# Optimization experiments

Measured on AMD Instinct MI355X. Metric: run time of the kernel, lower is better.

## Reference

```python
import jax, jax.numpy as jnp
import numpy as np


def _ln(x, g, b, eps=1e-5):
    m = jnp.mean(x, axis=-1, keepdims=True)
    v = jnp.var(x, axis=-1, keepdims=True)  # biased var, matches torch LayerNorm
    return (x - m) / jnp.sqrt(v + eps) * g + b


def setup_inputs() -> dict:
    key = jax.random.key(0)
    ks = jax.random.split(key, 10)
    B, S, T, D, F = 4, 8, 1024, 768, 16
    inp = {
        "target_hidden": jax.random.normal(ks[0], (B, T, D), jnp.float32),
        "support_hidden": jax.random.normal(ks[1], (B, S, T, D), jnp.float32),
        "support_token_mask": jax.random.bernoulli(ks[2], 0.8, (B, S, T)),
        "support_features": jax.random.normal(ks[3], (B, T, F), jnp.float32),
        # LayerNorm params
        "t_g": jnp.ones((D,), jnp.float32), "t_b": jnp.zeros((D,), jnp.float32),
        "s_g": jnp.ones((D,), jnp.float32), "s_b": jnp.zeros((D,), jnp.float32),
        "o_g": jnp.ones((D,), jnp.float32), "o_b": jnp.zeros((D,), jnp.float32),
        # score MLP: Linear(2D->D), GELU, Linear(D->1)
        "score_w1": jax.random.normal(ks[4], (2 * D, D), jnp.float32) * 0.02,
        "score_b1": jnp.zeros((D,), jnp.float32),
        "score_w2": jax.random.normal(ks[5], (D, 1), jnp.float32) * 0.02,
        "score_b2": jnp.zeros((1,), jnp.float32),
        # gate MLP: Linear(2D+F->D), GELU, Linear(D->1), Sigmoid
        "gate_w1": jax.random.normal(ks[6], (2 * D + F, D), jnp.float32) * 0.02,
        "gate_b1": jnp.zeros((D,), jnp.float32),
        "gate_w2": jax.random.normal(ks[7], (D, 1), jnp.float32) * 0.02,
        "gate_b2": jnp.zeros((1,), jnp.float32),
    }
    return inp


def reference(target_hidden, support_hidden, support_token_mask, support_features,
              t_g, t_b, s_g, s_b, o_g, o_b,
              score_w1, score_b1, score_w2, score_b2,
              gate_w1, gate_b1, gate_w2, gate_b2):
    D = target_hidden.shape[-1]
    mask = support_token_mask  # (B,S,T) bool

    th = _ln(target_hidden, t_g, t_b)        # (B,T,D)
    sh = _ln(support_hidden, s_g, s_b)       # (B,S,T,D)

    # score MLP on concat([target_expanded, support], -1) == split-weight form
    h = (jnp.einsum('btd,df->btf', th, score_w1[:D])[:, None, :, :]
         + jnp.einsum('bstd,df->bstf', sh, score_w1[D:]) + score_b1)  # (B,S,T,D)
    h = jax.nn.gelu(h, approximate=False)
    scores = jnp.einsum('bstd,d->bst', h, score_w2[:, 0]) + score_b2[0]  # (B,S,T)

    scores = jnp.where(mask, scores, -10000.0)
    w = jax.nn.softmax(scores, axis=1)
    w = w * mask.astype(w.dtype)
    w = w / jnp.clip(jnp.sum(w, axis=1, keepdims=True), 1e-8)

    summary = jnp.einsum('bst,bstd->btd', w, sh)  # (B,T,D)
    has_support = jnp.any(mask, axis=1)           # (B,T)
    summary = jnp.where(has_support[..., None], summary, 0.0)

    gcat = jnp.concatenate([th, summary, support_features], axis=-1)  # (B,T,2D+F)
    g = jax.nn.gelu(gcat @ gate_w1 + gate_b1, approximate=False)
    gate = jax.nn.sigmoid(g @ gate_w2 + gate_b2)  # (B,T,1)

    fused = gate * summary + (1.0 - gate) * th    # dropout is identity in eval
    out = _ln(th + fused, o_g, o_b)
    return out, gate.squeeze(-1)
```

## Files before the change

kernel.cpp:

```cpp
#include <hip/hip_runtime.h>
#include <hip/hip_bf16.h>

#define D768 768

typedef __attribute__((ext_vector_type(8))) short short8;
typedef __attribute__((ext_vector_type(4))) float f32x4;

__device__ __forceinline__ unsigned short f2bf(float f){
  union { float f; unsigned u; } v; v.f = f;
  unsigned r = v.u + 0x7FFFu + ((v.u >> 16) & 1u);
  return (unsigned short)(r >> 16);
}
__device__ __forceinline__ float bf2f(unsigned short u){
  union { unsigned u; float f; } v; v.u = ((unsigned)u) << 16;
  return v.f;
}
__device__ __forceinline__ float gelu_f(float x){
  float y = fabsf(x) * 0.7071067811865475f;
  float t = __builtin_amdgcn_rcpf(fmaf(0.3275911f, y, 1.0f));
  float p = fmaf(fmaf(fmaf(fmaf(1.061405429f, t, -1.453152027f), t, 1.421413741f),
                      t, -0.284496736f), t, 0.254829592f) * t;
  float e = __expf(-y * y);
  float erf_abs = fmaf(-p, e, 1.0f);
  float erfv = copysignf(erf_abs, x);
  return 0.5f * x * (1.0f + erfv);
}
__device__ __forceinline__ void gload16(const void* g, void* l){
  __builtin_amdgcn_global_load_lds((const __attribute__((address_space(1))) void*)g,
                                   (__attribute__((address_space(3))) void*)l, 16, 0, 0);
}

__global__ void k_ln(const float* __restrict__ x, const float* __restrict__ g,
                     const float* __restrict__ bia, float* __restrict__ of32,
                     unsigned short* __restrict__ obf, int ldo){
  int row = blockIdx.x;
  int t = threadIdx.x;
  const float* xr = x + (size_t)row * D768;
  float4 v = *(const float4*)(xr + t*4);
  float s  = v.x + v.y + v.z + v.w;
  float ss = v.x*v.x + v.y*v.y + v.z*v.z + v.w*v.w;
  for (int o = 32; o; o >>= 1){ s += __shfl_down(s, o); ss += __shfl_down(ss, o); }
  __shared__ float sb[6];
  int wid = t >> 6;
  if ((t & 63) == 0){ sb[wid] = s; sb[3+wid] = ss; }
  __syncthreads();
  s = sb[0] + sb[1] + sb[2]; ss = sb[3] + sb[4] + sb[5];
  float mean = s * (1.f/768.f);
  float var  = ss * (1.f/768.f) - mean*mean;
  float rstd = rsqrtf(var + 1e-5f);
  float4 gv = *(const float4*)(g + t*4);
  float4 bv = *(const float4*)(bia + t*4);
  float o0 = (v.x-mean)*rstd*gv.x + bv.x;
  float o1 = (v.y-mean)*rstd*gv.y + bv.y;
  float o2 = (v.z-mean)*rstd*gv.z + bv.z;
  float o3 = (v.w-mean)*rstd*gv.w + bv.w;
  if (of32){
    float4 ov; ov.x=o0; ov.y=o1; ov.z=o2; ov.w=o3;
    *(float4*)(of32 + (size_t)row * D768 + t*4) = ov;
  }
  ushort4 ub; ub.x=f2bf(o0); ub.y=f2bf(o1); ub.z=f2bf(o2); ub.w=f2bf(o3);
  *(ushort4*)(obf + (size_t)row * ldo + t*4) = ub;
}

__global__ void k_wtall(const float* __restrict__ sw1, const float* __restrict__ gw1,
                        unsigned short* __restrict__ WtA, unsigned short* __restrict__ WtB,
                        unsigned short* __restrict__ WtG,
                        float* __restrict__ scores, const float* __restrict__ sb2,
                        float* __restrict__ gacc, const float* __restrict__ gb2,
                        const unsigned char* __restrict__ m, int* __restrict__ flag){
  int blk = blockIdx.x;
  if (blk < 128){
    int i = blk * 256 + threadIdx.x;
    if (i < 32768) scores[i] = sb2[0];
    if (i < 4096)  gacc[i]   = gb2[0];
    if (blk == 0){
      __shared__ int s;
      if (threadIdx.x == 0) s = 0;
      __syncthreads();
      int nz = 0;
      for (int j = threadIdx.x; j < 2048; j += 256) nz += (m[4*j+1] != 0);
      atomicAdd(&s, nz);
      __syncthreads();
      if (threadIdx.x == 0) *flag = (s == 0) ? 1 : 0;
    }
    return;
  }
  int tile = blk - 128;
  const float* W; unsigned short* Wt; int Kin, Kpad;
  if (tile < 576)      { W = sw1;                 Wt = WtA; Kin = 768;  Kpad = 768;  }
  else if (tile < 1152){ W = sw1 + 768ull*768;    Wt = WtB; Kin = 768;  Kpad = 768;  tile -= 576; }
  else                 { W = gw1;                 Wt = WtG; Kin = 1552; Kpad = 1568; tile -= 1152; }
  int ntk = Kpad >> 5;
  int k0 = (tile % ntk) << 5, n0 = (tile / ntk) << 5;
  __shared__ float ts[32][33];
  int tx = threadIdx.x & 31, ty = threadIdx.x >> 5;
  #pragma unroll
  for (int r = 0; r < 4; ++r){
    int k = k0 + ty + r*8;
    ts[ty + r*8][tx] = (k < Kin) ? W[(size_t)k * D768 + n0 + tx] : 0.f;
  }
  __syncthreads();
  #pragma unroll
  for (int r = 0; r < 4; ++r){
    int n = n0 + ty + r*8;
    Wt[(size_t)n * Kpad + k0 + tx] = f2bf(ts[tx][ty + r*8]);
  }
}

template<int MODE, int BN>
__launch_bounds__(256)
__global__ void k_gemm(const unsigned short* __restrict__ A, int lda,
                       const unsigned short* __restrict__ Bt, int ldb,
                       int ksteps, int ntn,
                       const float* __restrict__ tproj,
                       const float* __restrict__ b1,
                       const float* __restrict__ w2,
                       float* __restrict__ out){
  constexpr int NJ  = BN / 32;
  constexpr int BCH = BN / 64;
  __shared__ __align__(16) unsigned short As[3][128*32];
  __shared__ __align__(16) unsigned short Bs[3][BN*32];
  const int cpx = gridDim.x >> 3;
  const int logical = ((int)blockIdx.x & 7) * cpx + ((int)blockIdx.x >> 3);
  const int m0 = (logical / ntn) * 128, n0 = (logical % ntn) * BN;
  const int t = threadIdx.x, lane = t & 63, w = t >> 6;
  const int wrow = (w >> 1) * 64, wcol = (w & 1) * (BN/2);
  const int lo16 = lane & 15;
  const int hs = ((lane >> 4) ^ ((lo16 >> 1) & 3)) * 8;
  const int crow = lane >> 2;
  const int cseg = (((lane & 3) ^ ((lane >> 3) & 3)) * 8);
  const unsigned short* ga = A  + (size_t)(m0 + w*32 + crow) * lda + cseg;
  const unsigned short* gb = Bt + (size_t)(n0 + w*(BN/4) + crow) * ldb + cseg;
  f32x4 acc[4][NJ] = {};

#define STAGEK(BUF, KS) do {                                                   \
    const unsigned short* gak_ = ga + (size_t)(KS)*32;                         \
    const unsigned short* gbk_ = gb + (size_t)(KS)*32;                         \
    _Pragma("unroll")                                                          \
    for (int c = 0; c < 2; ++c)                                                \
      gload16(gak_ + (size_t)(c*16)*lda, &As[BUF][w*1024 + c*512]);            \
    _Pragma("unroll")                                                          \
    for (int c = 0; c < BCH; ++c)                                              \
      gload16(gbk_ + (size_t)(c*16)*ldb, &Bs[BUF][w*(BN/4)*32 + c*512]);       \
  } while (0)

#define COMPUTEK(BUF) do {                                                     \
    const unsigned short* pa_ = &As[BUF][(wrow + lo16)*32 + hs];               \
    const unsigned short* pb_ = &Bs[BUF][(wcol + lo16)*32 + hs];               \
    short8 af_[4], bf_[NJ];                                                    \
    _Pragma("unroll")                                                          \
    for (int i = 0; i < 4; ++i) af_[i] = *(const short8*)(pa_ + i*16*32);      \
    _Pragma("unroll")                                                          \
    for (int j = 0; j < NJ; ++j) bf_[j] = *(const short8*)(pb_ + j*16*32);     \
    _Pragma("unroll")                                                          \
    for (int i = 0; i < 4; ++i)                                                \
      _Pragma("unroll")                                                        \
      for (int j = 0; j < NJ; ++j)                                             \
        acc[i][j] = __builtin_amdgcn_mfma_f32_16x16x32_bf16(af_[i], bf_[j], acc[i][j], 0, 0, 0); \
  } while (0)

#define WAITN(n) asm volatile("s_waitcnt vmcnt(" #n ")" ::: "memory")

  {
    int pro = ksteps < 2 ? ksteps : 2;
    for (int p = 0; p < pro; ++p) STAGEK(p, p);
  }
  for (int ks = 0; ks < ksteps; ++ks){
    int rem = ksteps - ks;
    if (rem >= 2){ if constexpr (BCH == 2) WAITN(4); else WAITN(3); }
    else WAITN(0);
    __builtin_amdgcn_s_barrier();
    __builtin_amdgcn_sched_barrier(0);
    if (ks + 2 < ksteps) STAGEK((ks + 2) % 3, ks + 2);
    COMPUTEK(ks % 3);
  }
#undef STAGEK
#undef COMPUTEK
#undef WAITN

  if (MODE == 0){
    #pragma unroll
    for (int i = 0; i < 4; ++i)
      #pragma unroll
      for (int reg = 0; reg < 4; ++reg){
        int row = m0 + wrow + i*16 + ((lane >> 4) << 2) + reg;
        float* orow = out + (size_t)row * D768 + n0 + wcol + (lane & 15);
        #pragma unroll
        for (int j = 0; j < NJ; ++j) orow[j*16] = acc[i][j][reg];
      }
  } else {
    #pragma unroll
    for (int i = 0; i < 4; ++i)
      #pragma unroll
      for (int reg = 0; reg < 4; ++reg){
        int row = m0 + wrow + i*16 + ((lane >> 4) << 2) + reg;
        const float* tp = nullptr;
        if (MODE == 1){
          int trow = ((row >> 13) << 10) | (row & 1023);
          tp = tproj + (size_t)trow * D768;
        }
        float contrib = 0.f;
        #pragma unroll
        for (int j = 0; j < NJ; ++j){
          int n = n0 + wcol + j*16 + (lane & 15);
          float v = acc[i][j][reg] + b1[n];
          if (MODE == 1) v += tp[n];
          contrib += gelu_f(v) * w2[n];
        }
        for (int o = 8; o; o >>= 1) contrib += __shfl_xor(contrib, o);
        if ((lane & 15) == 0) atomicAdd(&out[row], contrib);
      }
  }
}

__launch_bounds__(512)
__global__ void k_gemm8(const unsigned short* __restrict__ A, int lda,
                        const unsigned short* __restrict__ Bt, int ldb,
                        int ksteps, int ntn,
                        const float* __restrict__ tproj,
                        const float* __restrict__ b1,
                        const float* __restrict__ w2,
                        float* __restrict__ out){
  __shared__ __align__(16) unsigned short As[3][128*32];
  __shared__ __align__(16) unsigned short Bs[3][128*32];
  const int cpx = gridDim.x >> 3;
  const int logical = ((int)blockIdx.x & 7) * cpx + ((int)blockIdx.x >> 3);
  const int m0 = (logical / ntn) * 128, n0 = (logical % ntn) * 128;
  const int t = threadIdx.x, lane = t & 63, w = t >> 6;
  const int wrow = (w >> 2) * 64, wcol = (w & 3) * 32;
  const int lo16 = lane & 15;
  const int hs = ((lane >> 4) ^ ((lo16 >> 1) & 3)) * 8;
  const int crow = lane >> 2;
  const int cseg = (((lane & 3) ^ ((lane >> 3) & 3)) * 8);
  const unsigned short* ga = A  + (size_t)(m0 + w*16 + crow) * lda + cseg;
  const unsigned short* gb = Bt + (size_t)(n0 + w*16 + crow) * ldb + cseg;
  f32x4 acc[4][2] = {};

#define STAGEK(BUF, KS) do {                                                   \
    gload16(ga + (size_t)(KS)*32, &As[BUF][w*512]);                            \
    gload16(gb + (size_t)(KS)*32, &Bs[BUF][w*512]);                            \
  } while (0)

#define COMPUTEK(BUF) do {                                                     \
    const unsigned short* pa_ = &As[BUF][(wrow + lo16)*32 + hs];               \
    const unsigned short* pb_ = &Bs[BUF][(wcol + lo16)*32 + hs];               \
    short8 af_[4], bf_[2];                                                     \
    _Pragma("unroll")                                                          \
    for (int i = 0; i < 4; ++i) af_[i] = *(const short8*)(pa_ + i*16*32);      \
    _Pragma("unroll")                                                          \
    for (int j = 0; j < 2; ++j) bf_[j] = *(const short8*)(pb_ + j*16*32);      \
    _Pragma("unroll")                                                          \
    for (int i = 0; i < 4; ++i)                                                \
      _Pragma("unroll")                                                        \
      for (int j = 0; j < 2; ++j)                                              \
        acc[i][j] = __builtin_amdgcn_mfma_f32_16x16x32_bf16(af_[i], bf_[j], acc[i][j], 0, 0, 0); \
  } while (0)

#define WAITN(n) asm volatile("s_waitcnt vmcnt(" #n ")" ::: "memory")

  {
    int pro = ksteps < 2 ? ksteps : 2;
    for (int p = 0; p < pro; ++p) STAGEK(p, p);
  }
  for (int ks = 0; ks < ksteps; ++ks){
    int rem = ksteps - ks;
    if (rem >= 2) WAITN(2);
    else WAITN(0);
    __builtin_amdgcn_s_barrier();
    __builtin_amdgcn_sched_barrier(0);
    if (ks + 2 < ksteps) STAGEK((ks + 2) % 3, ks + 2);
    COMPUTEK(ks % 3);
  }
#undef STAGEK
#undef COMPUTEK
#undef WAITN

  #pragma unroll
  for (int i = 0; i < 4; ++i)
    #pragma unroll
    for (int reg = 0; reg < 4; ++reg){
      int row = m0 + wrow + i*16 + ((lane >> 4) << 2) + reg;
      int trow = ((row >> 13) << 10) | (row & 1023);
      const float* tp = tproj + (size_t)trow * D768;
      float contrib = 0.f;
      #pragma unroll
      for (int j = 0; j < 2; ++j){
        int n = n0 + wcol + j*16 + lo16;
        float v = acc[i][j][reg] + b1[n] + tp[n];
        contrib += gelu_f(v) * w2[n];
      }
      for (int o = 8; o; o >>= 1) contrib += __shfl_xor(contrib, o);
      if (lo16 == 0) atomicAdd(&out[row], contrib);
    }
}

__global__ void k_smx(const float* __restrict__ scores, const void* __restrict__ maskp,
                      const int* __restrict__ flag, const unsigned short* __restrict__ sh,
                      const float* __restrict__ feat,
                      unsigned short* __restrict__ gcat){
  int bt = blockIdx.x;
  int b = bt >> 10, tt = bt & 1023;
  int t = threadIdx.x;
  int f = *flag;
  float sc[8], mk[8];
  #pragma unroll
  for (int s = 0; s < 8; ++s){
    size_t idx = ((size_t)(b*8 + s) << 10) + tt;
    bool m = f ? (((const int*)maskp)[idx] != 0)
               : (((const unsigned char*)maskp)[idx] != 0);
    mk[s] = m ? 1.f : 0.f;
    float v = scores[idx];
    sc[s] = m ? v : -10000.f;
  }
  float mx = sc[0];
  #pragma unroll
  for (int s = 1; s < 8; ++s) mx = fmaxf(mx, sc[s]);
  float e[8], sum = 0.f;
  #pragma unroll
  for (int s = 0; s < 8; ++s){ e[s] = __expf(sc[s] - mx); sum += e[s]; }
  float inv = 1.f / sum;
  float wv[8], sum2 = 0.f;
  #pragma unroll
  for (int s = 0; s < 8; ++s){ wv[s] = e[s] * inv * mk[s]; sum2 += wv[s]; }
  float inv2 = 1.f / fmaxf(sum2, 1e-8f);
  #pragma unroll
  for (int s = 0; s < 8; ++s) wv[s] *= inv2;
  float a0=0.f, a1=0.f, a2=0.f, a3=0.f;
  #pragma unroll
  for (int s = 0; s < 8; ++s){
    const unsigned short* p = sh + (((size_t)(b*8+s) << 10) + tt) * D768 + t*4;
    ushort4 u = *(const ushort4*)p;
    float ws = wv[s];
    a0 += ws * bf2f(u.x); a1 += ws * bf2f(u.y); a2 += ws * bf2f(u.z); a3 += ws * bf2f(u.w);
  }
  ushort4 ub; ub.x=f2bf(a0); ub.y=f2bf(a1); ub.z=f2bf(a2); ub.w=f2bf(a3);
  *(ushort4*)(gcat + (size_t)bt * 1568 + 768 + t*4) = ub;
  if (t < 8){
    int c = 1536 + t*4;
    float4 fv = make_float4(0.f, 0.f, 0.f, 0.f);
    if (c < 1552) fv = *(const float4*)(feat + (size_t)bt * 16 + (c - 1536));
    ushort4 uf; uf.x=f2bf(fv.x); uf.y=f2bf(fv.y); uf.z=f2bf(fv.z); uf.w=f2bf(fv.w);
    *(ushort4*)(gcat + (size_t)bt * 1568 + c) = uf;
  }
}

__global__ void k_final(const float* __restrict__ th, const unsigned short* __restrict__ gcat,
                        const float* __restrict__ gacc, const float* __restrict__ og,
                        const float* __restrict__ ob, float* __restrict__ out,
                        float* __restrict__ outg){
  int r = blockIdx.x, t = threadIdx.x;
  float gv = 1.f / (1.f + __expf(-gacc[r]));
  if (t == 0) outg[r] = gv;
  float4 tv = *(const float4*)(th + (size_t)r * D768 + t*4);
  ushort4 su = *(const ushort4*)(gcat + (size_t)r * 1568 + 768 + t*4);
  float s0 = bf2f(su.x), s1 = bf2f(su.y), s2 = bf2f(su.z), s3 = bf2f(su.w);
  float x0 = (2.f-gv)*tv.x + gv*s0;
  float x1 = (2.f-gv)*tv.y + gv*s1;
  float x2 = (2.f-gv)*tv.z + gv*s2;
  float x3 = (2.f-gv)*tv.w + gv*s3;
  float s = x0+x1+x2+x3, ss = x0*x0+x1*x1+x2*x2+x3*x3;
  for (int o = 32; o; o >>= 1){ s += __shfl_down(s,o); ss += __shfl_down(ss,o); }
  __shared__ float sb[6];
  int wid = t >> 6;
  if ((t&63)==0){ sb[wid]=s; sb[3+wid]=ss; }
  __syncthreads();
  s = sb[0]+sb[1]+sb[2]; ss = sb[3]+sb[4]+sb[5];
  float mean = s*(1.f/768.f), var = ss*(1.f/768.f)-mean*mean;
  float rstd = rsqrtf(var + 1e-5f);
  float4 gvv = *(const float4*)(og + t*4);
  float4 bvv = *(const float4*)(ob + t*4);
  float4 ov;
  ov.x = (x0-mean)*rstd*gvv.x + bvv.x;
  ov.y = (x1-mean)*rstd*gvv.y + bvv.y;
  ov.z = (x2-mean)*rstd*gvv.z + bvv.z;
  ov.w = (x3-mean)*rstd*gvv.w + bvv.w;
  *(float4*)(out + (size_t)r * D768 + t*4) = ov;
}

extern "C" void kernel_launch(void* const* d_in, const int* in_sizes, int n_in,
                              void* d_out, int out_size, void* d_ws, size_t ws_size,
                              hipStream_t stream){
  const float* target = (const float*)d_in[0];
  const float* support= (const float*)d_in[1];
  const void*  maskp  = d_in[2];
  const float* feat   = (const float*)d_in[3];
  const float* t_g = (const float*)d_in[4];
  const float* t_b = (const float*)d_in[5];
  const float* s_g = (const float*)d_in[6];
  const float* s_b = (const float*)d_in[7];
  const float* o_g = (const float*)d_in[8];
  const float* o_b = (const float*)d_in[9];
  const float* sw1 = (const float*)d_in[10];
  const float* sb1 = (const float*)d_in[11];
  const float* sw2 = (const float*)d_in[12];
  const float* sb2 = (const float*)d_in[13];
  const float* gw1 = (const float*)d_in[14];
  const float* gb1 = (const float*)d_in[15];
  const float* gw2 = (const float*)d_in[16];
  const float* gb2 = (const float*)d_in[17];

  char* wsb = (char*)d_ws;
  size_t off = 0;
  auto alloc = [&](size_t bytes)->void*{
    void* p = wsb + off; off += (bytes + 255) & ~(size_t)255; return p;
  };
  float* th            = (float*)alloc(4096ull*768*4);
  unsigned short* sh   = (unsigned short*)alloc(32768ull*768*2);
  float* tproj         = (float*)alloc(4096ull*768*4);
  unsigned short* gcat = (unsigned short*)alloc(4096ull*1568*2);
  unsigned short* WtA  = (unsigned short*)alloc(768ull*768*2);
  unsigned short* WtB  = (unsigned short*)alloc(768ull*768*2);
  unsigned short* WtG  = (unsigned short*)alloc(768ull*1568*2);
  float* scores        = (float*)alloc(32768ull*4);
  float* gacc          = (float*)alloc(4096ull*4);
  int*   flag          = (int*)alloc(256);

  float* outm = (float*)d_out;
  float* outg = outm + 4096ull*768;

  k_wtall<<<2456, 256, 0, stream>>>(sw1, gw1, WtA, WtB, WtG,
                                    scores, sb2, gacc, gb2,
                                    (const unsigned char*)maskp, flag);
  k_ln<<<4096, 192, 0, stream>>>(target, t_g, t_b, th, gcat, 1568);
  k_gemm<0,64><<<384, 256, 0, stream>>>(gcat, 1568, WtA, 768, 24, 12,
                                        nullptr, nullptr, nullptr, tproj);
  k_ln<<<32768, 192, 0, stream>>>(support, s_g, s_b, (float*)nullptr, sh, 768);
  k_gemm8<<<1536, 512, 0, stream>>>(sh, 768, WtB, 768, 24, 6,
                                    tproj, sb1, sw2, scores);
  k_smx<<<4096, 192, 0, stream>>>(scores, maskp, flag, sh, feat, gcat);
  k_gemm<2,64><<<384, 256, 0, stream>>>(gcat, 1568, WtG, 1568, 49, 12,
                                        nullptr, gb1, gw2, gacc);
  k_final<<<4096, 192, 0, stream>>>(th, gcat, gacc, o_g, o_b, outm, outg);
}
```

Before: 180.7 us.

## Merge weight prep and both LayerNorms into one launch; new 8-wave gate GEMM

Weight transpose/convert, the score/gate accumulator init, and both LayerNorm passes (target and support) now run as one launch. Each LayerNorm block handles four rows with one wavefront per row, so the cross-wave shared-memory reduction and its barrier go away. The gate GEMM is replaced by a 512-thread, 8-wave kernel with a 128x64 tile, a 3-stage global-to-LDS pipeline and a fused GELU/w2 epilogue. This cuts launch count and tail effects and aims to raise occupancy of the gate GEMM, at the cost of a larger, more branchy kernel.

```diff
diff --git a/kernel.cpp b/kernel.cpp
--- a/kernel.cpp
+++ b/kernel.cpp
@@ -30,80 +30,95 @@
                                    (__attribute__((address_space(3))) void*)l, 16, 0, 0);
 }
 
-__global__ void k_ln(const float* __restrict__ x, const float* __restrict__ g,
-                     const float* __restrict__ bia, float* __restrict__ of32,
-                     unsigned short* __restrict__ obf, int ldo){
-  int row = blockIdx.x;
+__global__ __launch_bounds__(256)
+void k_mega(const float* __restrict__ target, const float* __restrict__ support,
+            const float* __restrict__ t_g, const float* __restrict__ t_b,
+            const float* __restrict__ s_g, const float* __restrict__ s_b,
+            float* __restrict__ th, unsigned short* __restrict__ gcat,
+            unsigned short* __restrict__ sh,
+            const float* __restrict__ sw1, const float* __restrict__ gw1,
+            unsigned short* __restrict__ WtA, unsigned short* __restrict__ WtB,
+            unsigned short* __restrict__ WtG,
+            float* __restrict__ scores, const float* __restrict__ sb2,
+            float* __restrict__ gacc, const float* __restrict__ gb2,
+            const unsigned char* __restrict__ m, int* __restrict__ flag){
+  int blk = blockIdx.x;
   int t = threadIdx.x;
-  const float* xr = x + (size_t)row * D768;
-  float4 v = *(const float4*)(xr + t*4);
-  float s  = v.x + v.y + v.z + v.w;
-  float ss = v.x*v.x + v.y*v.y + v.z*v.z + v.w*v.w;
-  for (int o = 32; o; o >>= 1){ s += __shfl_down(s, o); ss += __shfl_down(ss, o); }
-  __shared__ float sb[6];
-  int wid = t >> 6;
-  if ((t & 63) == 0){ sb[wid] = s; sb[3+wid] = ss; }
-  __syncthreads();
-  s = sb[0] + sb[1] + sb[2]; ss = sb[3] + sb[4] + sb[5];
-  float mean = s * (1.f/768.f);
-  float var  = ss * (1.f/768.f) - mean*mean;
-  float rstd = rsqrtf(var + 1e-5f);
-  float4 gv = *(const float4*)(g + t*4);
-  float4 bv = *(const float4*)(bia + t*4);
-  float o0 = (v.x-mean)*rstd*gv.x + bv.x;
-  float o1 = (v.y-mean)*rstd*gv.y + bv.y;
-  float o2 = (v.z-mean)*rstd*gv.z + bv.z;
-  float o3 = (v.w-mean)*rstd*gv.w + bv.w;
-  if (of32){
-    float4 ov; ov.x=o0; ov.y=o1; ov.z=o2; ov.w=o3;
-    *(float4*)(of32 + (size_t)row * D768 + t*4) = ov;
-  }
-  ushort4 ub; ub.x=f2bf(o0); ub.y=f2bf(o1); ub.z=f2bf(o2); ub.w=f2bf(o3);
-  *(ushort4*)(obf + (size_t)row * ldo + t*4) = ub;
-}
-
-__global__ void k_wtall(const float* __restrict__ sw1, const float* __restrict__ gw1,
-                        unsigned short* __restrict__ WtA, unsigned short* __restrict__ WtB,
-                        unsigned short* __restrict__ WtG,
-                        float* __restrict__ scores, const float* __restrict__ sb2,
-                        float* __restrict__ gacc, const float* __restrict__ gb2,
-                        const unsigned char* __restrict__ m, int* __restrict__ flag){
-  int blk = blockIdx.x;
   if (blk < 128){
-    int i = blk * 256 + threadIdx.x;
+    int i = blk * 256 + t;
     if (i < 32768) scores[i] = sb2[0];
     if (i < 4096)  gacc[i]   = gb2[0];
     if (blk == 0){
       __shared__ int s;
-      if (threadIdx.x == 0) s = 0;
+      if (t == 0) s = 0;
       __syncthreads();
       int nz = 0;
-      for (int j = threadIdx.x; j < 2048; j += 256) nz += (m[4*j+1] != 0);
+      for (int j = t; j < 2048; j += 256) nz += (m[4*j+1] != 0);
       atomicAdd(&s, nz);
       __syncthreads();
-      if (threadIdx.x == 0) *flag = (s == 0) ? 1 : 0;
+      if (t == 0) *flag = (s == 0) ? 1 : 0;
     }
     return;
   }
-  int tile = blk - 128;
-  const float* W; unsigned short* Wt; int Kin, Kpad;
-  if (tile < 576)      { W = sw1;                 Wt = WtA; Kin = 768;  Kpad = 768;  }
-  else if (tile < 1152){ W = sw1 + 768ull*768;    Wt = WtB; Kin = 768;  Kpad = 768;  tile -= 576; }
-  else                 { W = gw1;                 Wt = WtG; Kin = 1552; Kpad = 1568; tile -= 1152; }
-  int ntk = Kpad >> 5;
-  int k0 = (tile % ntk) << 5, n0 = (tile / ntk) << 5;
-  __shared__ float ts[32][33];
-  int tx = threadIdx.x & 31, ty = threadIdx.x >> 5;
-  #pragma unroll
-  for (int r = 0; r < 4; ++r){
-    int k = k0 + ty + r*8;
-    ts[ty + r*8][tx] = (k < Kin) ? W[(size_t)k * D768 + n0 + tx] : 0.f;
-  }
-  __syncthreads();
-  #pragma unroll
-  for (int r = 0; r < 4; ++r){
-    int n = n0 + ty + r*8;
-    Wt[(size_t)n * Kpad + k0 + tx] = f2bf(ts[tx][ty + r*8]);
+  if (blk < 2456){
+    int tile = blk - 128;
+    const float* W; unsigned short* Wt; int Kin, Kpad;
+    if (tile < 576)      { W = sw1;              Wt = WtA; Kin = 768;  Kpad = 768;  }
+    else if (tile < 1152){ W = sw1 + 768ull*768; Wt = WtB; Kin = 768;  Kpad = 768;  tile -= 576; }
+    else                 { W = gw1;              Wt = WtG; Kin = 1552; Kpad = 1568; tile -= 1152; }
+    int ntk = Kpad >> 5;
+    int k0 = (tile % ntk) << 5, n0 = (tile / ntk) << 5;
+    __shared__ float ts[32][33];
+    int tx = t & 31, ty = t >> 5;
+    #pragma unroll
+    for (int r = 0; r < 4; ++r){
+      int k = k0 + ty + r*8;
+      ts[ty + r*8][tx] = (k < Kin) ? W[(size_t)k * D768 + n0 + tx] : 0.f;
+    }
+    __syncthreads();
+    #pragma unroll
+    for (int r = 0; r < 4; ++r){
+      int n = n0 + ty + r*8;
+      Wt[(size_t)n * Kpad + k0 + tx] = f2bf(ts[tx][ty + r*8]);
+    }
+    return;
+  }
+  bool isT = blk < 3480;
+  int row = (isT ? (blk - 2456) : (blk - 3480)) * 4 + (t >> 6);
+  int lane = t & 63;
+  const float* xr = (isT ? target : support) + (size_t)row * D768;
+  float4 v0 = *(const float4*)(xr + lane*4);
+  float4 v1 = *(const float4*)(xr + 256 + lane*4);
+  float4 v2 = *(const float4*)(xr + 512 + lane*4);
+  float s  = v0.x+v0.y+v0.z+v0.w + v1.x+v1.y+v1.z+v1.w + v2.x+v2.y+v2.z+v2.w;
+  float ss = v0.x*v0.x+v0.y*v0.y+v0.z*v0.z+v0.w*v0.w
+           + v1.x*v1.x+v1.y*v1.y+v1.z*v1.z+v1.w*v1.w
+           + v2.x*v2.x+v2.y*v2.y+v2.z*v2.z+v2.w*v2.w;
+  #pragma unroll
+  for (int o = 32; o; o >>= 1){ s += __shfl_xor(s, o); ss += __shfl_xor(ss, o); }
+  float mean = s * (1.f/768.f);
+  float var  = ss * (1.f/768.f) - mean*mean;
+  float rstd = rsqrtf(var + 1e-5f);
+  const float* gg = isT ? t_g : s_g;
+  const float* bb = isT ? t_b : s_b;
+  #pragma unroll
+  for (int k = 0; k < 3; ++k){
+    int c = lane*4 + k*256;
+    float4 v = (k==0) ? v0 : (k==1) ? v1 : v2;
+    float4 gv = *(const float4*)(gg + c);
+    float4 bv = *(const float4*)(bb + c);
+    float o0 = (v.x-mean)*rstd*gv.x + bv.x;
+    float o1 = (v.y-mean)*rstd*gv.y + bv.y;
+    float o2 = (v.z-mean)*rstd*gv.z + bv.z;
+    float o3 = (v.w-mean)*rstd*gv.w + bv.w;
+    ushort4 ub; ub.x=f2bf(o0); ub.y=f2bf(o1); ub.z=f2bf(o2); ub.w=f2bf(o3);
+    if (isT){
+      float4 ov; ov.x=o0; ov.y=o1; ov.z=o2; ov.w=o3;
+      *(float4*)(th + (size_t)row * D768 + c) = ov;
+      *(ushort4*)(gcat + (size_t)row * 1568 + c) = ub;
+    } else {
+      *(ushort4*)(sh + (size_t)row * D768 + c) = ub;
+    }
   }
 }
 
@@ -294,6 +309,77 @@
     }
 }
 
+__launch_bounds__(512)
+__global__ void k_gemm8g(const unsigned short* __restrict__ A, int lda,
+                         const unsigned short* __restrict__ Bt, int ldb,
+                         int ksteps, int ntn,
+                         const float* __restrict__ b1,
+                         const float* __restrict__ w2,
+                         float* __restrict__ out){
+  __shared__ __align__(16) unsigned short As[3][128*32];
+  __shared__ __align__(16) unsigned short Bs[3][64*32];
+  const int cpx = gridDim.x >> 3;
+  const int logical = ((int)blockIdx.x & 7) * cpx + ((int)blockIdx.x >> 3);
+  const int m0 = (logical / ntn) * 128, n0 = (logical % ntn) * 64;
+  const int t = threadIdx.x, lane = t & 63, w = t >> 6;
+  const int wrow = (w >> 2) * 64, wcol = (w & 3) * 16;
+  const int lo16 = lane & 15;
+  const int hs = ((lane >> 4) ^ ((lo16 >> 1) & 3)) * 8;
+  const int crow = lane >> 2;
+  const int cseg = (((lane & 3) ^ ((lane >> 3) & 3)) * 8);
+  const unsigned short* ga = A  + (size_t)(m0 + w*16 + crow) * lda + cseg;
+  const unsigned short* gb = Bt + (size_t)(n0 + w*16 + crow) * ldb + cseg;
+  f32x4 acc[4] = {};
+
+#define STAGEK(BUF, KS) do {                                                   \
+    gload16(ga + (size_t)(KS)*32, &As[BUF][w*512]);                            \
+    if (w < 4) gload16(gb + (size_t)(KS)*32, &Bs[BUF][w*512]);                 \
+  } while (0)
+
+#define COMPUTEK(BUF) do {                                                     \
+    const unsigned short* pa_ = &As[BUF][(wrow + lo16)*32 + hs];               \
+    const unsigned short* pb_ = &Bs[BUF][(wcol + lo16)*32 + hs];               \
+    short8 af_[4], bf_;                                                        \
+    _Pragma("unroll")                                                          \
+    for (int i = 0; i < 4; ++i) af_[i] = *(const short8*)(pa_ + i*16*32);      \
+    bf_ = *(const short8*)pb_;                                                 \
+    _Pragma("unroll")                                                          \
+    for (int i = 0; i < 4; ++i)                                                \
+      acc[i] = __builtin_amdgcn_mfma_f32_16x16x32_bf16(af_[i], bf_, acc[i], 0, 0, 0); \
+  } while (0)
+
+#define WAITN(n) asm volatile("s_waitcnt vmcnt(" #n ")" ::: "memory")
+
+  {
+    int pro = ksteps < 2 ? ksteps : 2;
+    for (int p = 0; p < pro; ++p) STAGEK(p, p);
+  }
+  for (int ks = 0; ks < ksteps; ++ks){
+    int rem = ksteps - ks;
+    if (rem >= 2){ if (w < 4) WAITN(2); else WAITN(1); }
+    else WAITN(0);
+    __builtin_amdgcn_s_barrier();
+    __builtin_amdgcn_sched_barrier(0);
+    if (ks + 2 < ksteps) STAGEK((ks + 2) % 3, ks + 2);
+    COMPUTEK(ks % 3);
+  }
+#undef STAGEK
+#undef COMPUTEK
+#undef WAITN
+
+  #pragma unroll
+  for (int i = 0; i < 4; ++i)
+    #pragma unroll
+    for (int reg = 0; reg < 4; ++reg){
+      int row = m0 + wrow + i*16 + ((lane >> 4) << 2) + reg;
+      int n = n0 + wcol + lo16;
+      float v = acc[i][reg] + b1[n];
+      float contrib = gelu_f(v) * w2[n];
+      for (int o = 8; o; o >>= 1) contrib += __shfl_xor(contrib, o);
+      if (lo16 == 0) atomicAdd(&out[row], contrib);
+    }
+}
+
 __global__ void k_smx(const float* __restrict__ scores, const void* __restrict__ maskp,
                       const int* __restrict__ flag, const unsigned short* __restrict__ sh,
                       const float* __restrict__ feat,
@@ -418,17 +504,16 @@
   float* outm = (float*)d_out;
   float* outg = outm + 4096ull*768;
 
-  k_wtall<<<2456, 256, 0, stream>>>(sw1, gw1, WtA, WtB, WtG,
+  k_mega<<<11672, 256, 0, stream>>>(target, support, t_g, t_b, s_g, s_b,
+                                    th, gcat, sh, sw1, gw1, WtA, WtB, WtG,
                                     scores, sb2, gacc, gb2,
                                     (const unsigned char*)maskp, flag);
-  k_ln<<<4096, 192, 0, stream>>>(target, t_g, t_b, th, gcat, 1568);
   k_gemm<0,64><<<384, 256, 0, stream>>>(gcat, 1568, WtA, 768, 24, 12,
                                         nullptr, nullptr, nullptr, tproj);
-  k_ln<<<32768, 192, 0, stream>>>(support, s_g, s_b, (float*)nullptr, sh, 768);
   k_gemm8<<<1536, 512, 0, stream>>>(sh, 768, WtB, 768, 24, 6,
                                     tproj, sb1, sw2, scores);
   k_smx<<<4096, 192, 0, stream>>>(scores, maskp, flag, sh, feat, gcat);
-  k_gemm<2,64><<<384, 256, 0, stream>>>(gcat, 1568, WtG, 1568, 49, 12,
-                                        nullptr, gb1, gw2, gacc);
+  k_gemm8g<<<384, 512, 0, stream>>>(gcat, 1568, WtG, 1568, 49, 12,
+                                    gb1, gw2, gacc);
   k_final<<<4096, 192, 0, stream>>>(th, gcat, gacc, o_g, o_b, outm, outg);
 }
```

Measured after the change: 174.2 us. 3.6% less time.
